# Performance work log

Hardware: AMD Instinct MI355X
Metric: run time of the kernel (lower is better)

Reference implementation:

```python
import jax, jax.numpy as jnp
import numpy as np

T = 65536   # total tokens across all packed sequences
C = 768     # channels
K = 5       # kernel_size (odd)
NSEQ = 16   # number of packed sequences (>1 -> masked varlen path)


def setup_inputs() -> dict:
    key = jax.random.key(0)
    k1, k2, k3, k4 = jax.random.split(key, 4)
    x = jax.random.normal(k1, (T, C), dtype=jnp.float32)
    # cu_seqlens: [0, sorted interior boundaries, T]
    interior = jnp.sort(jax.random.randint(k2, (NSEQ - 1,), 1, T)).astype(jnp.int32)
    cu_seqlens = jnp.concatenate([
        jnp.zeros((1,), dtype=jnp.int32),
        interior,
        jnp.full((1,), T, dtype=jnp.int32),
    ])
    # depthwise conv weight [C, K] (== conv.weight[:, 0, :]) and bias [C]
    weight = jax.random.normal(k3, (C, K), dtype=jnp.float32) * 0.1
    bias = jax.random.normal(k4, (C,), dtype=jnp.float32) * 0.01
    return {"x": x, "cu_seqlens": cu_seqlens, "weight": weight, "bias": bias}


def reference(x, cu_seqlens, weight, bias):
    # Varlen Canon depthwise mixing with sequence-boundary masking.
    # x: [T, C] float32; cu_seqlens: [n_seqs+1] int32; weight: [C, K]; bias: [C].
    t = x.shape[0]
    radius = weight.shape[1] // 2
    positions = jnp.arange(t, dtype=cu_seqlens.dtype)
    # seq_id[i] = which packed sequence token i belongs to
    seq_id = jnp.searchsorted(cu_seqlens[1:], positions, side='right')
    out = jnp.zeros_like(x)
    for k, offset in enumerate(range(-radius, radius + 1)):  # K taps (small fixed loop)
        rolled_x = jnp.roll(x, -offset, axis=0)
        rolled_id = jnp.roll(seq_id, -offset, axis=0)
        valid = (rolled_id == seq_id)[:, None]               # [T, 1] boundary mask
        out = out + jnp.where(valid, rolled_x, 0.0) * weight[:, k]
    out = out + bias
    return x + out  # residual add
```

## Files before the change

### kernel.cpp

```cpp
#include <hip/hip_runtime.h>


#define CC  768
#define C4V (CC / 4)
#define KK  5
#define RR  2
#define TPB 32

typedef float nfloat4 __attribute__((ext_vector_type(4)));

__device__ __forceinline__ void nt_store(float4* p, const float4& v) {
    __builtin_nontemporal_store(*reinterpret_cast<const nfloat4*>(&v),
                                reinterpret_cast<nfloat4*>(p));
}

#define W(k, j) wl[(j) * KK + (k)]

__global__ __launch_bounds__(C4V, 4) void canon_dwconv_kernel(
    const float4* __restrict__ x4,
    const int*    __restrict__ cu,
    int nseq,
    const float4* __restrict__ w4,
    const float4* __restrict__ bias4,
    float4*       __restrict__ out4,
    int T)
{
    const int c4 = threadIdx.x;
    const int t0 = (int)blockIdx.x * TPB;

    float wl[KK * 4];
#pragma unroll
    for (int i = 0; i < KK; ++i) {
        const float4 v = w4[c4 * KK + i];
        wl[4 * i + 0] = v.x; wl[4 * i + 1] = v.y;
        wl[4 * i + 2] = v.z; wl[4 * i + 3] = v.w;
    }
    const float4 b = bias4[c4];

    int sid = 0;
    while (sid < nseq && cu[sid + 1] <= t0) ++sid;
    const int s0 = cu[sid];
    const int e0 = cu[sid + 1];

    const float4* __restrict__ xrow = x4 + c4;
    float4*       __restrict__ orow = out4 + c4;

    if (s0 <= t0 - RR && e0 >= t0 + TPB + RR) {
        float4 win[KK];
#pragma unroll
        for (int i = 0; i < KK - 1; ++i)
            win[i] = xrow[(size_t)(t0 - RR + i) * C4V];

#pragma unroll
        for (int tt = 0; tt < TPB; ++tt) {
            const int t = t0 + tt;
            win[(tt + KK - 1) % KK] = xrow[(size_t)(t + RR) * C4V];

            const float4 r0 = win[(tt + 0) % KK];
            const float4 r1 = win[(tt + 1) % KK];
            const float4 r2 = win[(tt + 2) % KK];
            const float4 r3 = win[(tt + 3) % KK];
            const float4 r4 = win[(tt + 4) % KK];

            float4 o;
            o.x = r2.x + b.x + r2.x * W(2,0)
                + r0.x * W(0,0) + r1.x * W(1,0)
                + r3.x * W(3,0) + r4.x * W(4,0);
            o.y = r2.y + b.y + r2.y * W(2,1)
                + r0.y * W(0,1) + r1.y * W(1,1)
                + r3.y * W(3,1) + r4.y * W(4,1);
            o.z = r2.z + b.z + r2.z * W(2,2)
                + r0.z * W(0,2) + r1.z * W(1,2)
                + r3.z * W(3,2) + r4.z * W(4,2);
            o.w = r2.w + b.w + r2.w * W(2,3)
                + r0.w * W(0,3) + r1.w * W(1,3)
                + r3.w * W(3,3) + r4.w * W(4,3);

            nt_store(&orow[(size_t)t * C4V], o);
        }
    } else {
        float4 win[KK];
#pragma unroll
        for (int i = 0; i < KK - 1; ++i) {
            int r  = t0 - RR + i;
            int rc = min(max(r, 0), T - 1);
            win[i] = xrow[(size_t)rc * C4V];
        }

#pragma unroll
        for (int tt = 0; tt < TPB; ++tt) {
            const int t = t0 + tt;
            if (t < T) {
                int rc = min(t + RR, T - 1);
                win[(tt + KK - 1) % KK] = xrow[(size_t)rc * C4V];

                while (sid < nseq && cu[sid + 1] <= t) ++sid;
                const int start = cu[sid];
                const int end   = cu[sid + 1];

                const float4 r0 = win[(tt + 0) % KK];
                const float4 r1 = win[(tt + 1) % KK];
                const float4 r2 = win[(tt + 2) % KK];
                const float4 r3 = win[(tt + 3) % KK];
                const float4 r4 = win[(tt + 4) % KK];

                const float m0 = (t - 2 >= start) ? 1.0f : 0.0f;
                const float m1 = (t - 1 >= start) ? 1.0f : 0.0f;
                const float m3 = (t + 1 <  end)  ? 1.0f : 0.0f;
                const float m4 = (t + 2 <  end)  ? 1.0f : 0.0f;

                float4 o;
                o.x = r2.x + b.x + r2.x * W(2,0)
                    + r0.x * (W(0,0) * m0) + r1.x * (W(1,0) * m1)
                    + r3.x * (W(3,0) * m3) + r4.x * (W(4,0) * m4);
                o.y = r2.y + b.y + r2.y * W(2,1)
                    + r0.y * (W(0,1) * m0) + r1.y * (W(1,1) * m1)
                    + r3.y * (W(3,1) * m3) + r4.y * (W(4,1) * m4);
                o.z = r2.z + b.z + r2.z * W(2,2)
                    + r0.z * (W(0,2) * m0) + r1.z * (W(1,2) * m1)
                    + r3.z * (W(3,2) * m3) + r4.z * (W(4,2) * m4);
                o.w = r2.w + b.w + r2.w * W(2,3)
                    + r0.w * (W(0,3) * m0) + r1.w * (W(1,3) * m1)
                    + r3.w * (W(3,3) * m3) + r4.w * (W(4,3) * m4);

                nt_store(&orow[(size_t)t * C4V], o);
            }
        }
    }
}

extern "C" void kernel_launch(void* const* d_in, const int* in_sizes, int n_in,
                              void* d_out, int out_size, void* d_ws, size_t ws_size,
                              hipStream_t stream) {
    const float4* x4     = (const float4*)d_in[0];
    const int*    cu     = (const int*)d_in[1];
    const float4* w4     = (const float4*)d_in[2];
    const float4* bias4  = (const float4*)d_in[3];
    float4*       out4   = (float4*)d_out;

    const int T    = in_sizes[0] / CC;
    const int nseq = in_sizes[1] - 1;

    const int grid = (T + TPB - 1) / TPB;
    canon_dwconv_kernel<<<grid, C4V, 0, stream>>>(x4, cu, nseq, w4, bias4, out4, T);
}
```

Before: 354.5 us.

## Use smaller row tiles with all loads issued upfront and plain stores

Cuts rows per block from 32 to 8 and loads the whole 12-row window into registers before computing, rather than streaming one row per output. It also drops the nontemporal stores in favour of normal stores and removes the occupancy hint from launch bounds. The aim is more memory-level parallelism per thread and more blocks in flight. In exchange the halo overhead rises from 36/32 to 12/8 rows read per block, which adds redundant global reads (partly absorbed by cache) and uses more registers.

```diff
diff --git a/kernel.cpp b/kernel.cpp
--- a/kernel.cpp
+++ b/kernel.cpp
@@ -1,22 +1,16 @@
 #include <hip/hip_runtime.h>
 
 
-#define CC  768
-#define C4V (CC / 4)
-#define KK  5
-#define RR  2
-#define TPB 32
-
-typedef float nfloat4 __attribute__((ext_vector_type(4)));
-
-__device__ __forceinline__ void nt_store(float4* p, const float4& v) {
-    __builtin_nontemporal_store(*reinterpret_cast<const nfloat4*>(&v),
-                                reinterpret_cast<nfloat4*>(p));
-}
+#define CC    768
+#define C4V   (CC / 4)
+#define KK    5
+#define RR    2
+#define TPB   8
+#define NROWS (TPB + 2 * RR)
 
 #define W(k, j) wl[(j) * KK + (k)]
 
-__global__ __launch_bounds__(C4V, 4) void canon_dwconv_kernel(
+__global__ __launch_bounds__(C4V) void canon_dwconv_kernel(
     const float4* __restrict__ x4,
     const int*    __restrict__ cu,
     int nseq,
@@ -46,21 +40,18 @@
     float4*       __restrict__ orow = out4 + c4;
 
     if (s0 <= t0 - RR && e0 >= t0 + TPB + RR) {
-        float4 win[KK];
+        float4 win[NROWS];
 #pragma unroll
-        for (int i = 0; i < KK - 1; ++i)
+        for (int i = 0; i < NROWS; ++i)
             win[i] = xrow[(size_t)(t0 - RR + i) * C4V];
 
 #pragma unroll
         for (int tt = 0; tt < TPB; ++tt) {
-            const int t = t0 + tt;
-            win[(tt + KK - 1) % KK] = xrow[(size_t)(t + RR) * C4V];
-
-            const float4 r0 = win[(tt + 0) % KK];
-            const float4 r1 = win[(tt + 1) % KK];
-            const float4 r2 = win[(tt + 2) % KK];
-            const float4 r3 = win[(tt + 3) % KK];
-            const float4 r4 = win[(tt + 4) % KK];
+            const float4 r0 = win[tt + 0];
+            const float4 r1 = win[tt + 1];
+            const float4 r2 = win[tt + 2];
+            const float4 r3 = win[tt + 3];
+            const float4 r4 = win[tt + 4];
 
             float4 o;
             o.x = r2.x + b.x + r2.x * W(2,0)
@@ -76,12 +67,12 @@
                 + r0.w * W(0,3) + r1.w * W(1,3)
                 + r3.w * W(3,3) + r4.w * W(4,3);
 
-            nt_store(&orow[(size_t)t * C4V], o);
+            orow[(size_t)(t0 + tt) * C4V] = o;
         }
     } else {
-        float4 win[KK];
+        float4 win[NROWS];
 #pragma unroll
-        for (int i = 0; i < KK - 1; ++i) {
+        for (int i = 0; i < NROWS; ++i) {
             int r  = t0 - RR + i;
             int rc = min(max(r, 0), T - 1);
             win[i] = xrow[(size_t)rc * C4V];
@@ -91,18 +82,15 @@
         for (int tt = 0; tt < TPB; ++tt) {
             const int t = t0 + tt;
             if (t < T) {
-                int rc = min(t + RR, T - 1);
-                win[(tt + KK - 1) % KK] = xrow[(size_t)rc * C4V];
-
                 while (sid < nseq && cu[sid + 1] <= t) ++sid;
                 const int start = cu[sid];
                 const int end   = cu[sid + 1];
 
-                const float4 r0 = win[(tt + 0) % KK];
-                const float4 r1 = win[(tt + 1) % KK];
-                const float4 r2 = win[(tt + 2) % KK];
-                const float4 r3 = win[(tt + 3) % KK];
-                const float4 r4 = win[(tt + 4) % KK];
+                const float4 r0 = win[tt + 0];
+                const float4 r1 = win[tt + 1];
+                const float4 r2 = win[tt + 2];
+                const float4 r3 = win[tt + 3];
+                const float4 r4 = win[tt + 4];
 
                 const float m0 = (t - 2 >= start) ? 1.0f : 0.0f;
                 const float m1 = (t - 1 >= start) ? 1.0f : 0.0f;
@@ -123,7 +111,7 @@
                     + r0.w * (W(0,3) * m0) + r1.w * (W(1,3) * m1)
                     + r3.w * (W(3,3) * m3) + r4.w * (W(4,3) * m4);
 
-                nt_store(&orow[(size_t)t * C4V], o);
+                orow[(size_t)t * C4V] = o;
             }
         }
     }
```

Result: faster. 335.2 us (-5.4%).
